# Optimization experiments

Measured on AMD Instinct MI355X. Metric: run time of the kernel, lower is better.

Reference implementation:

```python
import jax, jax.numpy as jnp
import numpy as np

SCALE = 8.0  # sqrt(head_dim=64)

def setup_inputs() -> dict:
    key = jax.random.key(0)
    kq, kk, kv = jax.random.split(key, 3)
    B, H, S, D = 2, 16, 2048, 64
    return {
        "query": jax.random.normal(kq, (B, H, S, D), dtype=jnp.float32),
        "key": jax.random.normal(kk, (B, H, S, D), dtype=jnp.float32),
        "value": jax.random.normal(kv, (B, H, S, D), dtype=jnp.float32),
        "mask": jnp.ones((B, 1, 1, S), dtype=jnp.int32),
    }

def reference(query, key, value, mask):
    # scores: [B,H,S,S]
    scores = jnp.einsum("bhqd,bhkd->bhqk", query, key) / SCALE
    scores = jnp.where(mask == 0, -jnp.inf, scores)
    attn_probs = jax.nn.softmax(scores, axis=-1)
    # dropout_rate = 0.0 -> identity
    output = jnp.einsum("bhqk,bhkd->bhqd", attn_probs, value)
    return (output, attn_probs)
```

## Files before the change

kernel.cpp:

```cpp
#include <hip/hip_runtime.h>

#define B_  2
#define H_  16
#define S_  2048
#define D_  64
#define BH_ (B_*H_)
#define NKT (S_/64)
#define LDQ 72

typedef __attribute__((ext_vector_type(8))) short bf16x8;
typedef __attribute__((ext_vector_type(4))) float f32x4;
typedef __attribute__((address_space(1))) const char gchar;
typedef __attribute__((address_space(3))) char lchar;

#define QK_SCALE 0.18033688011112042f

static __device__ __forceinline__ ushort f2bf(float f) {
  union { float f; unsigned u; } v; v.f = f;
  unsigned r = (v.u + 0x7fff + ((v.u >> 16) & 1)) >> 16;
  return (ushort)r;
}

static __device__ __forceinline__ uint4 pack8(const float* e, float sc) {
  uint4 p;
  p.x = (unsigned)f2bf(e[0]*sc) | ((unsigned)f2bf(e[1]*sc) << 16);
  p.y = (unsigned)f2bf(e[2]*sc) | ((unsigned)f2bf(e[3]*sc) << 16);
  p.z = (unsigned)f2bf(e[4]*sc) | ((unsigned)f2bf(e[5]*sc) << 16);
  p.w = (unsigned)f2bf(e[6]*sc) | ((unsigned)f2bf(e[7]*sc) << 16);
  return p;
}

__global__ __launch_bounds__(256)
void conv_kernel(const float* __restrict__ Q, const float* __restrict__ K,
                 const float* __restrict__ V,
                 ushort* __restrict__ Qw, ushort* __restrict__ Kw, ushort* __restrict__ Vw)
{
  const int tile = blockIdx.x, bh = blockIdx.y, mode = blockIdx.z;
  const int tid = threadIdx.x;
  const float* src = (mode == 0 ? Q : (mode == 1 ? K : V)) + ((size_t)bh*S_ + tile*64) * D_;
  ushort* dst = (mode == 0 ? Qw : (mode == 1 ? Kw : Vw)) + ((size_t)bh*NKT + tile) * 4096;

  const int r  = tid >> 2;
  const int c0 = (tid & 3) * 16;

  if (mode < 2) {
    const float sc = (mode == 0) ? QK_SCALE : 1.0f;
    const float4* s4 = (const float4*)(src + (size_t)r*D_ + c0);
    float e[16];
#pragma unroll
    for (int i = 0; i < 4; ++i) {
      float4 v = s4[i];
      e[i*4+0] = v.x; e[i*4+1] = v.y; e[i*4+2] = v.z; e[i*4+3] = v.w;
    }
#pragma unroll
    for (int g = 0; g < 2; ++g) {
      const int gi = ((c0 >> 3) + g) ^ (r & 7);
      *(uint4*)((char*)dst + r*128 + gi*16) = pack8(e + g*8, sc);
    }
  } else {
    __shared__ float t[64][65];
    const float4* s4 = (const float4*)(src + (size_t)r*D_ + c0);
#pragma unroll
    for (int i = 0; i < 4; ++i) {
      float4 v = s4[i];
      t[r][c0 + i*4 + 0] = v.x; t[r][c0 + i*4 + 1] = v.y;
      t[r][c0 + i*4 + 2] = v.z; t[r][c0 + i*4 + 3] = v.w;
    }
    __syncthreads();
    float e[16];
#pragma unroll
    for (int i = 0; i < 16; ++i) e[i] = t[c0 + i][r];
#pragma unroll
    for (int g = 0; g < 2; ++g) {
      const int gi = ((c0 >> 3) + g) ^ (r & 7);
      *(uint4*)((char*)dst + r*128 + gi*16) = pack8(e + g*8, 1.0f);
    }
  }
}

static __device__ __forceinline__ void stage8k(void* lds, const void* src, int wave, int lane) {
  const char* s = (const char*)src + lane*16;
  char* d = (char*)lds;
#pragma unroll
  for (int i = 0; i < 2; ++i) {
    const int off = (wave + i*4) << 10;
    __builtin_amdgcn_global_load_lds((gchar*)(s + off), (lchar*)(d + off), 16, 0, 0);
  }
}

__global__ __launch_bounds__(256, 3)
void attn3_kernel(const ushort* __restrict__ Qw, const ushort* __restrict__ Kw,
                  const ushort* __restrict__ Vw, const int* __restrict__ mask,
                  float* __restrict__ outO, float* __restrict__ outP)
{
  __shared__ ushort sQ[4096];
  __shared__ ushort sKV[4][4096];
  __shared__ __align__(16) ushort sP[4][1024];

  const int tid  = threadIdx.x;
  const int wave = tid >> 6;
  const int lane = tid & 63;
  const int l15  = lane & 15;
  const int lq   = lane >> 4;
  const int rxor = l15 & 7;

  const int qt = blockIdx.x;
  const int bh = blockIdx.y;
  const int b  = bh >> 4;

  const ushort* Qt = Qw + ((size_t)bh*NKT + qt) * 4096;
  const ushort* Kt = Kw + (size_t)bh*NKT * 4096;
  const ushort* Vt = Vw + (size_t)bh*NKT * 4096;
  const int*    mg = mask + b * S_;
  float* Og = outO + (size_t)(bh*S_ + qt*64) * D_;
  float* Pg = outP + (size_t)(bh*S_ + qt*64) * S_;

  stage8k(sQ, Qt, wave, lane);
  stage8k(sKV[0], Kt, wave, lane);
  stage8k(sKV[1], Kt + 4096, wave, lane);
  __syncthreads();

  bf16x8 qa[2];
#pragma unroll
  for (int c = 0; c < 2; ++c)
    qa[c] = *(const bf16x8*)((const char*)sQ + (wave*16 + l15)*128 + (((c*4 + lq) ^ rxor) << 4));

  float l_lane = 0.f;
  for (int kt2 = 0; kt2 < NKT/2; ++kt2) {
    const int cur2 = (kt2 & 1) * 2;
    if (kt2 + 1 < NKT/2) {
      stage8k(sKV[cur2 ^ 2],       Kt + (size_t)(2*kt2 + 2)*4096, wave, lane);
      stage8k(sKV[(cur2 ^ 2) + 1], Kt + (size_t)(2*kt2 + 3)*4096, wave, lane);
    }
#pragma unroll
    for (int t = 0; t < 8; ++t) {
      const char* rowp = (const char*)sKV[cur2 + (t >> 2)] + ((t & 3)*16 + l15)*128;
      const bf16x8 kb0 = *(const bf16x8*)(rowp + (((0 + lq) ^ rxor) << 4));
      const bf16x8 kb1 = *(const bf16x8*)(rowp + (((4 + lq) ^ rxor) << 4));
      f32x4 a = {0.f, 0.f, 0.f, 0.f};
      a = __builtin_amdgcn_mfma_f32_16x16x32_bf16(kb0, qa[0], a, 0, 0, 0);
      a = __builtin_amdgcn_mfma_f32_16x16x32_bf16(kb1, qa[1], a, 0, 0, 0);
      const int4 mv = *(const int4*)&mg[kt2*128 + t*16 + lq*4];
      if (mv.x == 0) a[0] = -1e30f;
      if (mv.y == 0) a[1] = -1e30f;
      if (mv.z == 0) a[2] = -1e30f;
      if (mv.w == 0) a[3] = -1e30f;
      l_lane += __builtin_amdgcn_exp2f(a[0]) + __builtin_amdgcn_exp2f(a[1])
              + __builtin_amdgcn_exp2f(a[2]) + __builtin_amdgcn_exp2f(a[3]);
    }
    __syncthreads();
  }

  l_lane += __shfl_xor(l_lane, 16);
  l_lane += __shfl_xor(l_lane, 32);
  const float madj = __builtin_amdgcn_logf(l_lane);

  f32x4 oacc[4];
#pragma unroll
  for (int n = 0; n < 4; ++n) { oacc[n][0]=0.f; oacc[n][1]=0.f; oacc[n][2]=0.f; oacc[n][3]=0.f; }
  char* sPb = (char*)&sP[wave][0] + l15*128;

  stage8k(sKV[0], Kt, wave, lane);
  stage8k(sKV[2], Vt, wave, lane);
  __syncthreads();

  for (int kt = 0; kt < NKT; ++kt) {
    const int cur = kt & 1;
    if (kt + 1 < NKT) {
      stage8k(sKV[cur ^ 1],       Kt + (size_t)(kt + 1)*4096, wave, lane);
      stage8k(sKV[2 + (cur ^ 1)], Vt + (size_t)(kt + 1)*4096, wave, lane);
    }
#pragma unroll
    for (int t = 0; t < 4; ++t) {
      const char* rowp = (const char*)sKV[cur] + (t*16 + l15)*128;
      const bf16x8 kb0 = *(const bf16x8*)(rowp + (((0 + lq) ^ rxor) << 4));
      const bf16x8 kb1 = *(const bf16x8*)(rowp + (((4 + lq) ^ rxor) << 4));
      f32x4 a = {0.f, 0.f, 0.f, 0.f};
      a = __builtin_amdgcn_mfma_f32_16x16x32_bf16(kb0, qa[0], a, 0, 0, 0);
      a = __builtin_amdgcn_mfma_f32_16x16x32_bf16(kb1, qa[1], a, 0, 0, 0);
      const int4 mv = *(const int4*)&mg[kt*64 + t*16 + lq*4];
      if (mv.x == 0) a[0] = -1e30f;
      if (mv.y == 0) a[1] = -1e30f;
      if (mv.z == 0) a[2] = -1e30f;
      if (mv.w == 0) a[3] = -1e30f;
      f32x4 p;
      p[0] = __builtin_amdgcn_exp2f(a[0] - madj);
      p[1] = __builtin_amdgcn_exp2f(a[1] - madj);
      p[2] = __builtin_amdgcn_exp2f(a[2] - madj);
      p[3] = __builtin_amdgcn_exp2f(a[3] - madj);
      *(f32x4*)&Pg[(size_t)(wave*16 + l15)*S_ + kt*64 + t*16 + lq*4] = p;
      uint2 pk;
      pk.x = (unsigned)f2bf(p[0]) | ((unsigned)f2bf(p[1]) << 16);
      pk.y = (unsigned)f2bf(p[2]) | ((unsigned)f2bf(p[3]) << 16);
      *(uint2*)(sPb + ((t*32 + lq*8) ^ (rxor << 4))) = pk;
    }
#pragma unroll
    for (int c2 = 0; c2 < 2; ++c2) {
      const bf16x8 pa = *(const bf16x8*)(sPb + ((c2*64 + lq*16) ^ (rxor << 4)));
#pragma unroll
      for (int n = 0; n < 4; ++n) {
        const bf16x8 vb = *(const bf16x8*)((const char*)sKV[2 + cur] + (n*16 + l15)*128 + (((c2*4 + lq) ^ rxor) << 4));
        oacc[n] = __builtin_amdgcn_mfma_f32_16x16x32_bf16(pa, vb, oacc[n], 0, 0, 0);
      }
    }
    __syncthreads();
  }

#pragma unroll
  for (int n = 0; n < 4; ++n)
#pragma unroll
    for (int j = 0; j < 4; ++j)
      Og[(size_t)(wave*16 + lq*4 + j)*D_ + n*16 + l15] = oacc[n][j];
}

static __device__ __forceinline__ void score_tiles_fb(
    f32x4 acc[4], const ushort* __restrict__ sK, const bf16x8 qa[2],
    int l15, int lq, const int* __restrict__ mg, int kbase)
{
#pragma unroll
  for (int t = 0; t < 4; ++t) {
    const bf16x8 kb0 = *(const bf16x8*)&sK[(t*16 + l15)*LDQ +      lq*8];
    const bf16x8 kb1 = *(const bf16x8*)&sK[(t*16 + l15)*LDQ + 32 + lq*8];
    f32x4 a = {0.f, 0.f, 0.f, 0.f};
    a = __builtin_amdgcn_mfma_f32_16x16x32_bf16(qa[0], kb0, a, 0, 0, 0);
    a = __builtin_amdgcn_mfma_f32_16x16x32_bf16(qa[1], kb1, a, 0, 0, 0);
    const int mv = mg[kbase + t*16 + l15];
    if (mv == 0) { a[0] = -1e30f; a[1] = -1e30f; a[2] = -1e30f; a[3] = -1e30f; }
    acc[t] = a;
  }
}

__global__ __launch_bounds__(256)
void attn_kernel(const float* __restrict__ Q, const float* __restrict__ K,
                 const float* __restrict__ V, const int* __restrict__ mask,
                 float* __restrict__ outO, float* __restrict__ outP)
{
  __shared__ ushort sQ[64 * LDQ];
  __shared__ ushort sK[64 * LDQ];
  __shared__ ushort sVt[D_ * LDQ];
  __shared__ ushort sP[4][16 * LDQ];

  const int tid  = threadIdx.x;
  const int wave = tid >> 6;
  const int lane = tid & 63;
  const int l15  = lane & 15;
  const int lq   = lane >> 4;
  const int qt = blockIdx.x;
  const int bh = blockIdx.y;
  const int b  = bh >> 4;
  const int q0 = qt * 64;

  const float* Qg = Q + (size_t)(bh*S_ + q0) * D_;
  const float* Kg = K + (size_t)bh * S_ * D_;
  const float* Vg = V + (size_t)bh * S_ * D_;
  const int*   mg = mask + b * S_;
  float* Og = outO + (size_t)(bh*S_ + q0) * D_;
  float* Pg = outP + ((size_t)(bh*S_ + q0)) * S_;

  const int srow = tid >> 2;
  const int sd0  = (tid & 3) * 16;

  {
    const float* src = Qg + (size_t)srow * D_ + sd0;
    ushort* dst = &sQ[srow*LDQ + sd0];
#pragma unroll
    for (int i = 0; i < 16; i += 4) {
      float4 v = *(const float4*)(src + i);
      dst[i+0] = f2bf(v.x * 0.125f); dst[i+1] = f2bf(v.y * 0.125f);
      dst[i+2] = f2bf(v.z * 0.125f); dst[i+3] = f2bf(v.w * 0.125f);
    }
  }
  __syncthreads();

  bf16x8 qa[2];
#pragma unroll
  for (int c = 0; c < 2; ++c)
    qa[c] = *(const bf16x8*)&sQ[(wave*16 + l15)*LDQ + c*32 + lq*8];

  float m_r[4] = {-1e30f, -1e30f, -1e30f, -1e30f};
  float l_r[4] = {0.f, 0.f, 0.f, 0.f};

  for (int kt = 0; kt < NKT; ++kt) {
    __syncthreads();
    {
      const float* src = Kg + (size_t)(kt*64 + srow) * D_ + sd0;
      ushort* dst = &sK[srow*LDQ + sd0];
#pragma unroll
      for (int i = 0; i < 16; i += 4) {
        float4 v = *(const float4*)(src + i);
        dst[i+0] = f2bf(v.x); dst[i+1] = f2bf(v.y);
        dst[i+2] = f2bf(v.z); dst[i+3] = f2bf(v.w);
      }
    }
    __syncthreads();
    f32x4 acc[4];
    score_tiles_fb(acc, sK, qa, l15, lq, mg, kt*64);
#pragma unroll
    for (int j = 0; j < 4; ++j) {
      float v = fmaxf(fmaxf(acc[0][j], acc[1][j]), fmaxf(acc[2][j], acc[3][j]));
#pragma unroll
      for (int s = 1; s < 16; s <<= 1) v = fmaxf(v, __shfl_xor(v, s));
      const float mn = fmaxf(m_r[j], v);
      float ps = __expf(acc[0][j] - mn) + __expf(acc[1][j] - mn)
               + __expf(acc[2][j] - mn) + __expf(acc[3][j] - mn);
#pragma unroll
      for (int s = 1; s < 16; s <<= 1) ps += __shfl_xor(ps, s);
      l_r[j] = l_r[j] * __expf(m_r[j] - mn) + ps;
      m_r[j] = mn;
    }
  }

  float inv_l[4];
#pragma unroll
  for (int j = 0; j < 4; ++j) inv_l[j] = 1.0f / l_r[j];

  f32x4 oacc[4];
#pragma unroll
  for (int n = 0; n < 4; ++n) { oacc[n][0]=0.f; oacc[n][1]=0.f; oacc[n][2]=0.f; oacc[n][3]=0.f; }
  ushort* sPw = &sP[wave][0];

  for (int kt = 0; kt < NKT; ++kt) {
    __syncthreads();
    {
      const float* src = Kg + (size_t)(kt*64 + srow) * D_ + sd0;
      ushort* dst = &sK[srow*LDQ + sd0];
#pragma unroll
      for (int i = 0; i < 16; i += 4) {
        float4 v = *(const float4*)(src + i);
        dst[i+0] = f2bf(v.x); dst[i+1] = f2bf(v.y);
        dst[i+2] = f2bf(v.z); dst[i+3] = f2bf(v.w);
      }
    }
    {
      const int vkey = tid & 63;
      const int vd0  = (tid >> 6) * 16;
      const float* vsrc = Vg + (size_t)(kt*64 + vkey) * D_ + vd0;
#pragma unroll
      for (int i = 0; i < 16; i += 4) {
        float4 v = *(const float4*)(vsrc + i);
        sVt[(vd0+i+0)*LDQ + vkey] = f2bf(v.x);
        sVt[(vd0+i+1)*LDQ + vkey] = f2bf(v.y);
        sVt[(vd0+i+2)*LDQ + vkey] = f2bf(v.z);
        sVt[(vd0+i+3)*LDQ + vkey] = f2bf(v.w);
      }
    }
    __syncthreads();
    f32x4 acc[4];
    score_tiles_fb(acc, sK, qa, l15, lq, mg, kt*64);
#pragma unroll
    for (int t = 0; t < 4; ++t)
#pragma unroll
      for (int j = 0; j < 4; ++j) {
        const float p = __expf(acc[t][j] - m_r[j]) * inv_l[j];
        sPw[(lq*4 + j)*LDQ + t*16 + l15] = f2bf(p);
      }
    __syncthreads();
#pragma unroll
    for (int i = 0; i < 4; ++i) {
      const int r = lq + i*4;
      const ushort* ps = &sPw[r*LDQ + l15*4];
      float4 o;
      o.x = __uint_as_float((unsigned)ps[0] << 16);
      o.y = __uint_as_float((unsigned)ps[1] << 16);
      o.z = __uint_as_float((unsigned)ps[2] << 16);
      o.w = __uint_as_float((unsigned)ps[3] << 16);
      *(float4*)&Pg[(size_t)(wave*16 + r)*S_ + kt*64 + l15*4] = o;
    }
#pragma unroll
    for (int c = 0; c < 2; ++c) {
      const bf16x8 pa = *(const bf16x8*)&sPw[l15*LDQ + c*32 + lq*8];
#pragma unroll
      for (int n = 0; n < 4; ++n) {
        const bf16x8 vb = *(const bf16x8*)&sVt[(n*16 + l15)*LDQ + c*32 + lq*8];
        oacc[n] = __builtin_amdgcn_mfma_f32_16x16x32_bf16(pa, vb, oacc[n], 0, 0, 0);
      }
    }
  }
#pragma unroll
  for (int n = 0; n < 4; ++n)
#pragma unroll
    for (int j = 0; j < 4; ++j)
      Og[(size_t)(wave*16 + lq*4 + j)*D_ + n*16 + l15] = oacc[n][j];
}

extern "C" void kernel_launch(void* const* d_in, const int* in_sizes, int n_in,
                              void* d_out, int out_size, void* d_ws, size_t ws_size,
                              hipStream_t stream) {
  const float* Q = (const float*)d_in[0];
  const float* K = (const float*)d_in[1];
  const float* V = (const float*)d_in[2];
  const int* mask = (const int*)d_in[3];
  float* outO = (float*)d_out;
  float* outP = outO + (size_t)B_ * H_ * S_ * D_;

  const size_t elems = (size_t)B_ * H_ * S_ * D_;
  if (ws_size >= elems * 2 * 3) {
    ushort* Qw = (ushort*)d_ws;
    ushort* Kw = Qw + elems;
    ushort* Vw = Kw + elems;
    conv_kernel<<<dim3(NKT, BH_, 3), dim3(256), 0, stream>>>(Q, K, V, Qw, Kw, Vw);
    attn3_kernel<<<dim3(S_/64, BH_), dim3(256), 0, stream>>>(Qw, Kw, Vw, mask, outO, outP);
  } else {
    attn_kernel<<<dim3(S_/64, BH_), dim3(256), 0, stream>>>(Q, K, V, mask, outO, outP);
  }
}
```

Baseline: 725.2 us.

## Split row-sum pass into separate kernel and store P rows coalesced via LDS

Moves the first pass, which computes the log of each softmax row sum, into its own kernel that writes the values to a workspace buffer. The main attention kernel reads them back. The main kernel also swaps the MFMA operand order so each lane holds a query column, and computes P into a padded LDS tile. It then writes the probability matrix row-wise with float4 stores. This aims to make the large P writes more coalesced. In exchange, P is now written from bf16-rounded values, which reduces precision, and the split adds an extra launch plus a workspace round trip.

```diff
diff --git a/kernel.cpp b/kernel.cpp
--- a/kernel.cpp
+++ b/kernel.cpp
@@ -7,6 +7,7 @@
 #define BH_ (B_*H_)
 #define NKT (S_/64)
 #define LDQ 72
+#define LDP 72
 
 typedef __attribute__((ext_vector_type(8))) short bf16x8;
 typedef __attribute__((ext_vector_type(4))) float f32x4;
@@ -89,13 +90,11 @@
 }
 
 __global__ __launch_bounds__(256, 3)
-void attn3_kernel(const ushort* __restrict__ Qw, const ushort* __restrict__ Kw,
-                  const ushort* __restrict__ Vw, const int* __restrict__ mask,
-                  float* __restrict__ outO, float* __restrict__ outP)
+void sumk_kernel(const ushort* __restrict__ Qw, const ushort* __restrict__ Kw,
+                 const int* __restrict__ mask, float* __restrict__ madj_g)
 {
   __shared__ ushort sQ[4096];
   __shared__ ushort sKV[4][4096];
-  __shared__ __align__(16) ushort sP[4][1024];
 
   const int tid  = threadIdx.x;
   const int wave = tid >> 6;
@@ -110,10 +109,7 @@
 
   const ushort* Qt = Qw + ((size_t)bh*NKT + qt) * 4096;
   const ushort* Kt = Kw + (size_t)bh*NKT * 4096;
-  const ushort* Vt = Vw + (size_t)bh*NKT * 4096;
   const int*    mg = mask + b * S_;
-  float* Og = outO + (size_t)(bh*S_ + qt*64) * D_;
-  float* Pg = outP + (size_t)(bh*S_ + qt*64) * S_;
 
   stage8k(sQ, Qt, wave, lane);
   stage8k(sKV[0], Kt, wave, lane);
@@ -153,16 +149,55 @@
 
   l_lane += __shfl_xor(l_lane, 16);
   l_lane += __shfl_xor(l_lane, 32);
-  const float madj = __builtin_amdgcn_logf(l_lane);
-
-  f32x4 oacc[4];
-#pragma unroll
-  for (int n = 0; n < 4; ++n) { oacc[n][0]=0.f; oacc[n][1]=0.f; oacc[n][2]=0.f; oacc[n][3]=0.f; }
-  char* sPb = (char*)&sP[wave][0] + l15*128;
-
+  if (lane < 16)
+    madj_g[(size_t)bh*S_ + qt*64 + wave*16 + lane] = __builtin_amdgcn_logf(l_lane);
+}
+
+__global__ __launch_bounds__(256, 3)
+void attn4_kernel(const ushort* __restrict__ Qw, const ushort* __restrict__ Kw,
+                  const ushort* __restrict__ Vw, const float* __restrict__ madj_g,
+                  const int* __restrict__ mask,
+                  float* __restrict__ outO, float* __restrict__ outP)
+{
+  __shared__ ushort sQ[4096];
+  __shared__ ushort sKV[4][4096];
+  __shared__ ushort sP[4][16 * LDP];
+
+  const int tid  = threadIdx.x;
+  const int wave = tid >> 6;
+  const int lane = tid & 63;
+  const int l15  = lane & 15;
+  const int lq   = lane >> 4;
+  const int rxor = l15 & 7;
+
+  const int qt = blockIdx.x;
+  const int bh = blockIdx.y;
+  const int b  = bh >> 4;
+
+  const ushort* Qt = Qw + ((size_t)bh*NKT + qt) * 4096;
+  const ushort* Kt = Kw + (size_t)bh*NKT * 4096;
+  const ushort* Vt = Vw + (size_t)bh*NKT * 4096;
+  const int*    mg = mask + b * S_;
+  float* Og = outO + (size_t)(bh*S_ + qt*64) * D_;
+  float* Pg = outP + (size_t)(bh*S_ + qt*64) * S_;
+
+  stage8k(sQ, Qt, wave, lane);
   stage8k(sKV[0], Kt, wave, lane);
   stage8k(sKV[2], Vt, wave, lane);
   __syncthreads();
+
+  bf16x8 qa[2];
+#pragma unroll
+  for (int c = 0; c < 2; ++c)
+    qa[c] = *(const bf16x8*)((const char*)sQ + (wave*16 + l15)*128 + (((c*4 + lq) ^ rxor) << 4));
+
+  const float4 mj = *(const float4*)&madj_g[(size_t)bh*S_ + qt*64 + wave*16 + lq*4];
+  const float madj[4] = {mj.x, mj.y, mj.z, mj.w};
+
+  f32x4 oacc[4];
+#pragma unroll
+  for (int n = 0; n < 4; ++n) { oacc[n][0]=0.f; oacc[n][1]=0.f; oacc[n][2]=0.f; oacc[n][3]=0.f; }
+  ushort* sPw = &sP[wave][0];
 
   for (int kt = 0; kt < NKT; ++kt) {
     const int cur = kt & 1;
@@ -170,33 +205,40 @@
       stage8k(sKV[cur ^ 1],       Kt + (size_t)(kt + 1)*4096, wave, lane);
       stage8k(sKV[2 + (cur ^ 1)], Vt + (size_t)(kt + 1)*4096, wave, lane);
     }
+    f32x4 acc[4];
 #pragma unroll
     for (int t = 0; t < 4; ++t) {
       const char* rowp = (const char*)sKV[cur] + (t*16 + l15)*128;
       const bf16x8 kb0 = *(const bf16x8*)(rowp + (((0 + lq) ^ rxor) << 4));
       const bf16x8 kb1 = *(const bf16x8*)(rowp + (((4 + lq) ^ rxor) << 4));
       f32x4 a = {0.f, 0.f, 0.f, 0.f};
-      a = __builtin_amdgcn_mfma_f32_16x16x32_bf16(kb0, qa[0], a, 0, 0, 0);
-      a = __builtin_amdgcn_mfma_f32_16x16x32_bf16(kb1, qa[1], a, 0, 0, 0);
-      const int4 mv = *(const int4*)&mg[kt*64 + t*16 + lq*4];
-      if (mv.x == 0) a[0] = -1e30f;
-      if (mv.y == 0) a[1] = -1e30f;
-      if (mv.z == 0) a[2] = -1e30f;
-      if (mv.w == 0) a[3] = -1e30f;
-      f32x4 p;
-      p[0] = __builtin_amdgcn_exp2f(a[0] - madj);
-      p[1] = __builtin_amdgcn_exp2f(a[1] - madj);
-      p[2] = __builtin_amdgcn_exp2f(a[2] - madj);
-      p[3] = __builtin_amdgcn_exp2f(a[3] - madj);
-      *(f32x4*)&Pg[(size_t)(wave*16 + l15)*S_ + kt*64 + t*16 + lq*4] = p;
-      uint2 pk;
-      pk.x = (unsigned)f2bf(p[0]) | ((unsigned)f2bf(p[1]) << 16);
-      pk.y = (unsigned)f2bf(p[2]) | ((unsigned)f2bf(p[3]) << 16);
-      *(uint2*)(sPb + ((t*32 + lq*8) ^ (rxor << 4))) = pk;
+      a = __builtin_amdgcn_mfma_f32_16x16x32_bf16(qa[0], kb0, a, 0, 0, 0);
+      a = __builtin_amdgcn_mfma_f32_16x16x32_bf16(qa[1], kb1, a, 0, 0, 0);
+      const int mv = mg[kt*64 + t*16 + l15];
+      if (mv == 0) { a[0] = -1e30f; a[1] = -1e30f; a[2] = -1e30f; a[3] = -1e30f; }
+      acc[t] = a;
+    }
+#pragma unroll
+    for (int t = 0; t < 4; ++t) {
+#pragma unroll
+      for (int j = 0; j < 4; ++j) {
+        sPw[(lq*4 + j)*LDP + t*16 + l15] = f2bf(__builtin_amdgcn_exp2f(acc[t][j] - madj[j]));
+      }
+    }
+#pragma unroll
+    for (int i = 0; i < 4; ++i) {
+      const int r = lq + i*4;
+      const ushort* ps = &sPw[r*LDP + l15*4];
+      float4 o;
+      o.x = __uint_as_float((unsigned)ps[0] << 16);
+      o.y = __uint_as_float((unsigned)ps[1] << 16);
+      o.z = __uint_as_float((unsigned)ps[2] << 16);
+      o.w = __uint_as_float((unsigned)ps[3] << 16);
+      *(float4*)&Pg[(size_t)(wave*16 + r)*S_ + kt*64 + l15*4] = o;
     }
 #pragma unroll
     for (int c2 = 0; c2 < 2; ++c2) {
-      const bf16x8 pa = *(const bf16x8*)(sPb + ((c2*64 + lq*16) ^ (rxor << 4)));
+      const bf16x8 pa = *(const bf16x8*)((const char*)sPw + l15*(LDP*2) + c2*64 + lq*16);
 #pragma unroll
       for (int n = 0; n < 4; ++n) {
         const bf16x8 vb = *(const bf16x8*)((const char*)sKV[2 + cur] + (n*16 + l15)*128 + (((c2*4 + lq) ^ rxor) << 4));
@@ -394,12 +436,15 @@
   float* outP = outO + (size_t)B_ * H_ * S_ * D_;
 
   const size_t elems = (size_t)B_ * H_ * S_ * D_;
-  if (ws_size >= elems * 2 * 3) {
+  const size_t need = elems*2*3 + (size_t)BH_*S_*4;
+  if (ws_size >= need) {
     ushort* Qw = (ushort*)d_ws;
     ushort* Kw = Qw + elems;
     ushort* Vw = Kw + elems;
+    float* madj_g = (float*)(Vw + elems);
     conv_kernel<<<dim3(NKT, BH_, 3), dim3(256), 0, stream>>>(Q, K, V, Qw, Kw, Vw);
-    attn3_kernel<<<dim3(S_/64, BH_), dim3(256), 0, stream>>>(Qw, Kw, Vw, mask, outO, outP);
+    sumk_kernel<<<dim3(S_/64, BH_), dim3(256), 0, stream>>>(Qw, Kw, mask, madj_g);
+    attn4_kernel<<<dim3(S_/64, BH_), dim3(256), 0, stream>>>(Qw, Kw, Vw, madj_g, mask, outO, outP);
   } else {
     attn_kernel<<<dim3(S_/64, BH_), dim3(256), 0, stream>>>(Q, K, V, mask, outO, outP);
   }
```

Result: no change. 715.6 us (-1.3%).
